# Kernel tuning notes

Measured on AMD Instinct MI355X. Metric: run time of the kernel, lower is better.

Reference implementation:

```python
import jax, jax.numpy as jnp
import numpy as np

D = 1024      # input_size
H = 16        # num_heads
HD = D // H   # head_dim
B, S = 8, 1024


def setup_inputs() -> dict:
    key = jax.random.key(0)
    ks = jax.random.split(key, 9)
    s = 1.0 / np.sqrt(D)
    return {
        "x": jax.random.normal(ks[0], (B, S, D), dtype=jnp.float32),
        "Wq": jax.random.uniform(ks[1], (D, D), jnp.float32, -s, s),
        "bq": jax.random.uniform(ks[2], (D,), jnp.float32, -s, s),
        "Wk": jax.random.uniform(ks[3], (D, D), jnp.float32, -s, s),
        "bk": jax.random.uniform(ks[4], (D,), jnp.float32, -s, s),
        "Wv": jax.random.uniform(ks[5], (D, D), jnp.float32, -s, s),
        "bv": jax.random.uniform(ks[6], (D,), jnp.float32, -s, s),
        "Wf": jax.random.uniform(ks[7], (D, D), jnp.float32, -s, s),
        "bf": jax.random.uniform(ks[8], (D,), jnp.float32, -s, s),
    }


def reference(x, Wq, bq, Wk, bk, Wv, bv, Wf, bf):
    b, s, d = x.shape
    # torch Linear: x @ W.T + b; split into heads -> [b, H, s, HD]
    def split(y):
        return y.reshape(b, s, H, HD).transpose(0, 2, 1, 3)
    q = split(x @ Wq.T + bq)
    k = split(x @ Wk.T + bk)
    v = split(x @ Wv.T + bv)
    scores = jnp.einsum("bhqd,bhkd->bhqk", q, k) / jnp.sqrt(jnp.float32(HD))
    probs = jax.nn.softmax(scores, axis=-1)
    ctx = jnp.einsum("bhqk,bhkd->bhqd", probs, v)
    ctx = ctx.transpose(0, 2, 1, 3).reshape(b, s, d)
    out = ctx @ Wf.T + bf
    return (out, probs)
```

## Files before the change

### kernel.cpp

```cpp
#include <hip/hip_runtime.h>

typedef __bf16 bf16;
typedef __bf16 bf16x4 __attribute__((ext_vector_type(4)));
typedef __bf16 bf16x8 __attribute__((ext_vector_type(8)));
typedef float  f32x4  __attribute__((ext_vector_type(4)));

constexpr int Bb = 8, Ss = 1024, Dd = 1024, Hh = 16, HDd = 64;
constexpr int Mm = Bb * Ss;
constexpr int Kk = 1024;

struct CastArgs {
  const float* src[5];
  bf16* dst[5];
  int cum[5];
};
__global__ void cast_all(CastArgs a, int tot) {
  int i = blockIdx.x * blockDim.x + threadIdx.x;
  if (i >= tot) return;
  int s, base;
  if (i < a.cum[0])      { s = 0; base = 0; }
  else if (i < a.cum[1]) { s = 1; base = a.cum[0]; }
  else if (i < a.cum[2]) { s = 2; base = a.cum[1]; }
  else if (i < a.cum[3]) { s = 3; base = a.cum[2]; }
  else                   { s = 4; base = a.cum[3]; }
  int j = i - base;
  float4 v = reinterpret_cast<const float4*>(a.src[s])[j];
  bf16x4 o = { (bf16)v.x, (bf16)v.y, (bf16)v.z, (bf16)v.w };
  reinterpret_cast<bf16x4*>(a.dst[s])[j] = o;
}

__device__ __forceinline__ void gemm_loop(const bf16* __restrict__ A, const bf16* __restrict__ Bm,
                                          int bm, int bn, unsigned char* As, unsigned char* Bs,
                                          int w, int lane, int l15, int g, f32x4 (&acc)[4][4]) {
  const int wr = (w >> 1) * 64, wc = (w & 1) * 64;
  (void)wr; (void)wc;
  const bf16* srcA[4];
  const bf16* srcB[4];
#pragma unroll
  for (int i = 0; i < 4; ++i) {
    int gch = (w * 4 + i) * 64 + lane;
    int r = gch >> 3, c = gch & 7, cs = c ^ (r & 7);
    srcA[i] = A  + (size_t)(bm * 128 + r) * Kk + cs * 8;
    srcB[i] = Bm + (size_t)(bn * 128 + r) * Kk + cs * 8;
  }
  for (int kt = 0; kt < Kk / 64; ++kt) {
    __syncthreads();
#pragma unroll
    for (int i = 0; i < 4; ++i) {
      __builtin_amdgcn_global_load_lds(
          (const __attribute__((address_space(1))) void*)(srcA[i] + kt * 64),
          (__attribute__((address_space(3))) void*)(As + (w * 4 + i) * 1024), 16, 0, 0);
      __builtin_amdgcn_global_load_lds(
          (const __attribute__((address_space(1))) void*)(srcB[i] + kt * 64),
          (__attribute__((address_space(3))) void*)(Bs + (w * 4 + i) * 1024), 16, 0, 0);
    }
    __syncthreads();
#pragma unroll
    for (int kk = 0; kk < 2; ++kk) {
      const int kb = kk * 64 + g * 16;
      bf16x8 af[4], bfr[4];
#pragma unroll
      for (int mi = 0; mi < 4; ++mi) {
        int row = ((w >> 1) * 64) + mi * 16 + l15;
        af[mi] = *reinterpret_cast<const bf16x8*>(As + row * 128 + (kb ^ ((row & 7) << 4)));
      }
#pragma unroll
      for (int ni = 0; ni < 4; ++ni) {
        int row = ((w & 1) * 64) + ni * 16 + l15;
        bfr[ni] = *reinterpret_cast<const bf16x8*>(Bs + row * 128 + (kb ^ ((row & 7) << 4)));
      }
#pragma unroll
      for (int mi = 0; mi < 4; ++mi)
#pragma unroll
        for (int ni = 0; ni < 4; ++ni)
          acc[mi][ni] = __builtin_amdgcn_mfma_f32_16x16x32_bf16(af[mi], bfr[ni], acc[mi][ni], 0, 0, 0);
    }
  }
}

__global__ __launch_bounds__(256) void gemm_qkv(const bf16* __restrict__ x,
                                                const bf16* __restrict__ wq, const bf16* __restrict__ wk,
                                                const bf16* __restrict__ wv,
                                                const float* __restrict__ bq, const float* __restrict__ bk,
                                                const float* __restrict__ bv,
                                                bf16* __restrict__ Qo, bf16* __restrict__ Ko,
                                                bf16* __restrict__ Vto) {
  const int tid = threadIdx.x;
  const int lane = tid & 63;
  const int w = tid >> 6;
  const int l15 = lane & 15, g = lane >> 4;
  const int z = blockIdx.z;

  const bf16* A; const bf16* Bm; int bm, bn;
  if (z < 2) { A = x; Bm = z ? wk : wq; bm = blockIdx.x; bn = blockIdx.y; }
  else       { A = wv; Bm = x;          bm = blockIdx.y; bn = blockIdx.x; }

  __shared__ __align__(16) unsigned char As[128 * 128];
  __shared__ __align__(16) unsigned char Bs[128 * 128];
  f32x4 acc[4][4] = {};
  gemm_loop(A, Bm, bm, bn, As, Bs, w, lane, l15, g, acc);

  const int wr = (w >> 1) * 64, wc = (w & 1) * 64;
  if (z < 2) {
    const float* bias = z ? bk : bq;
    bf16* out = z ? Ko : Qo;
    const float scale = z ? 1.f : 0.125f;
#pragma unroll
    for (int ni = 0; ni < 4; ++ni) {
      int col = bn * 128 + wc + ni * 16 + l15;
      float bv_ = bias[col];
#pragma unroll
      for (int mi = 0; mi < 4; ++mi)
#pragma unroll
        for (int r = 0; r < 4; ++r) {
          int row = bm * 128 + wr + mi * 16 + g * 4 + r;
          float val = (acc[mi][ni][r] + bv_) * scale;
          size_t adr = ((size_t)((row >> 10) * Hh + (col >> 6)) * Ss + (row & 1023)) * HDd + (col & 63);
          out[adr] = (bf16)val;
        }
    }
  } else {
#pragma unroll
    for (int mi = 0; mi < 4; ++mi)
#pragma unroll
      for (int r = 0; r < 4; ++r) {
        int row = bm * 128 + wr + mi * 16 + g * 4 + r;
        float bv_ = bv[row];
#pragma unroll
        for (int ni = 0; ni < 4; ++ni) {
          int col = bn * 128 + wc + ni * 16 + l15;
          size_t adr = ((size_t)((col >> 10) * Hh + (row >> 6)) * HDd + (row & 63)) * Ss + (col & 1023);
          Vto[adr] = (bf16)(acc[mi][ni][r] + bv_);
        }
      }
  }
}

__global__ __launch_bounds__(256) void gemm_out(const bf16* __restrict__ A, const bf16* __restrict__ Bm,
                                                const float* __restrict__ bias, float* __restrict__ out) {
  const int tid = threadIdx.x;
  const int lane = tid & 63;
  const int w = tid >> 6;
  const int l15 = lane & 15, g = lane >> 4;
  const int bn = blockIdx.x, bm = blockIdx.y;
  __shared__ __align__(16) unsigned char As[128 * 128];
  __shared__ __align__(16) unsigned char Bs[128 * 128];
  f32x4 acc[4][4] = {};
  gemm_loop(A, Bm, bm, bn, As, Bs, w, lane, l15, g, acc);
  const int wr = (w >> 1) * 64, wc = (w & 1) * 64;
#pragma unroll
  for (int ni = 0; ni < 4; ++ni) {
    int col = bn * 128 + wc + ni * 16 + l15;
    float bv_ = bias[col];
#pragma unroll
    for (int mi = 0; mi < 4; ++mi)
#pragma unroll
      for (int r = 0; r < 4; ++r) {
        int row = bm * 128 + wr + mi * 16 + g * 4 + r;
        out[(size_t)row * Dd + col] = acc[mi][ni][r] + bv_;
      }
  }
}

__global__ __launch_bounds__(512) void attn_fused(const bf16* __restrict__ Q,
                                                  const bf16* __restrict__ Kt,
                                                  const bf16* __restrict__ Vt,
                                                  float* __restrict__ probs,
                                                  bf16* __restrict__ ctx) {
  const int tid = threadIdx.x;
  const int lane = tid & 63;
  const int w = tid >> 6;
  const int l15 = lane & 15, g = lane >> 4;
  const int bh = blockIdx.x >> 3;
  const int qt = blockIdx.x & 7;
  const int q0 = qt * 128 + w * 16;

  __shared__ __align__(16) unsigned char Ks[128 * 128];
  __shared__ __align__(16) unsigned char Vs[64 * 256];
  __shared__ __align__(16) bf16 Ps[8][16][40];

  bf16x8 qf0, qf1;
  {
    const bf16* qp = Q + ((size_t)bh * Ss + q0 + l15) * HDd + g * 8;
    qf0 = *reinterpret_cast<const bf16x8*>(qp);
    qf1 = *reinterpret_cast<const bf16x8*>(qp + 32);
  }
  const bf16* kbase = Kt + (size_t)bh * Ss * HDd;
  const bf16* vbase = Vt + (size_t)bh * HDd * Ss;

  const bf16* ksrc[2];
  const bf16* vsrc[2];
#pragma unroll
  for (int i = 0; i < 2; ++i) {
    int chunk = i * 512 + tid;
    int kr = chunk >> 3, kc = (chunk & 7) ^ (kr & 7);
    ksrc[i] = kbase + (size_t)kr * HDd + kc * 8;
    int vr = chunk >> 4, vc = (chunk & 15) ^ (vr & 15);
    vsrc[i] = vbase + (size_t)vr * Ss + vc * 8;
  }

  auto kread = [&](int nk, int half) -> bf16x8 {
    int row = nk * 16 + l15;
    int chunk = (half * 4 + g) ^ (row & 7);
    return *reinterpret_cast<const bf16x8*>(Ks + row * 128 + chunk * 16);
  };
  auto vread = [&](int ni, int nkp) -> bf16x8 {
    int row = ni * 16 + l15;
    int chunk = (nkp * 4 + g) ^ (row & 15);
    return *reinterpret_cast<const bf16x8*>(Vs + row * 256 + chunk * 16);
  };

  float lr[4] = {0.f, 0.f, 0.f, 0.f};

  for (int kt = 0; kt < 8; ++kt) {
    __syncthreads();
#pragma unroll
    for (int i = 0; i < 2; ++i)
      __builtin_amdgcn_global_load_lds(
          (const __attribute__((address_space(1))) void*)(ksrc[i] + kt * 128 * HDd),
          (__attribute__((address_space(3))) void*)(Ks + (i * 512 + w * 64) * 16), 16, 0, 0);
    __syncthreads();
#pragma unroll
    for (int nk = 0; nk < 8; ++nk) {
      f32x4 sc = {0.f, 0.f, 0.f, 0.f};
      sc = __builtin_amdgcn_mfma_f32_16x16x32_bf16(qf0, kread(nk, 0), sc, 0, 0, 0);
      sc = __builtin_amdgcn_mfma_f32_16x16x32_bf16(qf1, kread(nk, 1), sc, 0, 0, 0);
#pragma unroll
      for (int r = 0; r < 4; ++r) lr[r] += __expf(sc[r]);
    }
  }
#pragma unroll
  for (int r = 0; r < 4; ++r) {
#pragma unroll
    for (int off = 1; off < 16; off <<= 1) lr[r] += __shfl_xor(lr[r], off, 64);
  }
  float rl[4];
#pragma unroll
  for (int r = 0; r < 4; ++r) rl[r] = 1.f / lr[r];

  float* prow[4];
#pragma unroll
  for (int r = 0; r < 4; ++r) prow[r] = probs + ((size_t)bh * Ss + q0 + g * 4 + r) * Ss;

  f32x4 cacc[4] = {};

  for (int kt = 0; kt < 8; ++kt) {
    __syncthreads();
#pragma unroll
    for (int i = 0; i < 2; ++i) {
      __builtin_amdgcn_global_load_lds(
          (const __attribute__((address_space(1))) void*)(ksrc[i] + kt * 128 * HDd),
          (__attribute__((address_space(3))) void*)(Ks + (i * 512 + w * 64) * 16), 16, 0, 0);
      __builtin_amdgcn_global_load_lds(
          (const __attribute__((address_space(1))) void*)(vsrc[i] + kt * 128),
          (__attribute__((address_space(3))) void*)(Vs + (i * 512 + w * 64) * 16), 16, 0, 0);
    }
    __syncthreads();
#pragma unroll
    for (int nkp = 0; nkp < 4; ++nkp) {
#pragma unroll
      for (int h = 0; h < 2; ++h) {
        int nk = nkp * 2 + h;
        f32x4 sc = {0.f, 0.f, 0.f, 0.f};
        sc = __builtin_amdgcn_mfma_f32_16x16x32_bf16(qf0, kread(nk, 0), sc, 0, 0, 0);
        sc = __builtin_amdgcn_mfma_f32_16x16x32_bf16(qf1, kread(nk, 1), sc, 0, 0, 0);
#pragma unroll
        for (int r = 0; r < 4; ++r) {
          float p = __expf(sc[r]) * rl[r];
          prow[r][kt * 128 + nk * 16 + l15] = p;
          Ps[w][g * 4 + r][h * 16 + l15] = (bf16)p;
        }
      }
      bf16x8 pf = *reinterpret_cast<const bf16x8*>(&Ps[w][l15][g * 8]);
#pragma unroll
      for (int ni = 0; ni < 4; ++ni)
        cacc[ni] = __builtin_amdgcn_mfma_f32_16x16x32_bf16(pf, vread(ni, nkp), cacc[ni], 0, 0, 0);
    }
  }

  const int bb = bh >> 4, hh = bh & 15;
#pragma unroll
  for (int ni = 0; ni < 4; ++ni)
#pragma unroll
    for (int r = 0; r < 4; ++r) {
      int q = q0 + g * 4 + r;
      ctx[((size_t)bb * Ss + q) * Dd + hh * 64 + ni * 16 + l15] = (bf16)cacc[ni][r];
    }
}

extern "C" void kernel_launch(void* const* d_in, const int* in_sizes, int n_in,
                              void* d_out, int out_size, void* d_ws, size_t ws_size,
                              hipStream_t stream) {
  (void)in_sizes; (void)n_in; (void)out_size; (void)ws_size;
  const float* x   = (const float*)d_in[0];
  const float* Wq  = (const float*)d_in[1];
  const float* bq  = (const float*)d_in[2];
  const float* Wk  = (const float*)d_in[3];
  const float* bk  = (const float*)d_in[4];
  const float* Wv  = (const float*)d_in[5];
  const float* bv  = (const float*)d_in[6];
  const float* Wf  = (const float*)d_in[7];
  const float* bfp = (const float*)d_in[8];

  char* ws = (char*)d_ws;
  size_t off = 0;
  auto alloc = [&](size_t n) { void* p = ws + off; off += (n + 255) & ~(size_t)255; return p; };
  bf16* xb   = (bf16*)alloc((size_t)Mm * Dd * 2);
  bf16* wqb  = (bf16*)alloc((size_t)Dd * Dd * 2);
  bf16* wkb  = (bf16*)alloc((size_t)Dd * Dd * 2);
  bf16* wvb  = (bf16*)alloc((size_t)Dd * Dd * 2);
  bf16* wfb  = (bf16*)alloc((size_t)Dd * Dd * 2);
  bf16* Qb   = (bf16*)alloc((size_t)Mm * Dd * 2);
  bf16* Kb   = (bf16*)alloc((size_t)Mm * Dd * 2);
  bf16* Vtb  = (bf16*)alloc((size_t)Mm * Dd * 2);
  bf16* ctxb = (bf16*)alloc((size_t)Mm * Dd * 2);

  CastArgs ca;
  ca.src[0] = x;  ca.dst[0] = xb;  int n0 = Mm * Dd / 4;
  ca.src[1] = Wq; ca.dst[1] = wqb; int nw = Dd * Dd / 4;
  ca.src[2] = Wk; ca.dst[2] = wkb;
  ca.src[3] = Wv; ca.dst[3] = wvb;
  ca.src[4] = Wf; ca.dst[4] = wfb;
  ca.cum[0] = n0; ca.cum[1] = n0 + nw; ca.cum[2] = n0 + 2 * nw;
  ca.cum[3] = n0 + 3 * nw; ca.cum[4] = n0 + 4 * nw;
  int tot = ca.cum[4];
  cast_all<<<(tot + 255) / 256, 256, 0, stream>>>(ca, tot);

  gemm_qkv<<<dim3(Mm / 128, Dd / 128, 3), 256, 0, stream>>>(xb, wqb, wkb, wvb, bq, bk, bv, Qb, Kb, Vtb);

  float* probs = (float*)d_out + (size_t)Mm * Dd;
  attn_fused<<<dim3(Bb * Hh * 8), 512, 0, stream>>>(Qb, Kb, Vtb, probs, ctxb);

  gemm_out<<<dim3(Dd / 128, Mm / 128), 256, 0, stream>>>(ctxb, wfb, bfp, (float*)d_out);
}
```

Baseline: 284.8 us.

## Double-buffer K tiles, transpose score MFMA, vectorize prob stores, read V directly

The attention kernel now double-buffers the K tile in LDS, prefetching the next tile while computing on the current one, and runs the second pass in reverse order so the last K tile from pass one is reused. The score MFMA operands are swapped so each lane holds four consecutive keys for one query row. This allows float4 stores of probabilities and bf16x4 writes into the P scratch, and reduces the row-sum reduction to two shuffles. V is no longer staged in LDS; it is loaded straight from global memory per MFMA, which saves LDS and barriers but may add global latency.

```diff
diff --git a/kernel.cpp b/kernel.cpp
--- a/kernel.cpp
+++ b/kernel.cpp
@@ -32,8 +32,6 @@
 __device__ __forceinline__ void gemm_loop(const bf16* __restrict__ A, const bf16* __restrict__ Bm,
                                           int bm, int bn, unsigned char* As, unsigned char* Bs,
                                           int w, int lane, int l15, int g, f32x4 (&acc)[4][4]) {
-  const int wr = (w >> 1) * 64, wc = (w & 1) * 64;
-  (void)wr; (void)wc;
   const bf16* srcA[4];
   const bf16* srcB[4];
 #pragma unroll
@@ -175,8 +173,7 @@
   const int qt = blockIdx.x & 7;
   const int q0 = qt * 128 + w * 16;
 
-  __shared__ __align__(16) unsigned char Ks[128 * 128];
-  __shared__ __align__(16) unsigned char Vs[64 * 256];
+  __shared__ __align__(16) unsigned char Ks[2][128 * 128];
   __shared__ __align__(16) bf16 Ps[8][16][40];
 
   bf16x8 qf0, qf1;
@@ -189,94 +186,83 @@
   const bf16* vbase = Vt + (size_t)bh * HDd * Ss;
 
   const bf16* ksrc[2];
-  const bf16* vsrc[2];
 #pragma unroll
   for (int i = 0; i < 2; ++i) {
     int chunk = i * 512 + tid;
     int kr = chunk >> 3, kc = (chunk & 7) ^ (kr & 7);
     ksrc[i] = kbase + (size_t)kr * HDd + kc * 8;
-    int vr = chunk >> 4, vc = (chunk & 15) ^ (vr & 15);
-    vsrc[i] = vbase + (size_t)vr * Ss + vc * 8;
-  }
-
-  auto kread = [&](int nk, int half) -> bf16x8 {
+  }
+
+#define STAGE_K(buf, kt)                                                                   \
+  {                                                                                        \
+    _Pragma("unroll") for (int i = 0; i < 2; ++i)                                          \
+        __builtin_amdgcn_global_load_lds(                                                  \
+            (const __attribute__((address_space(1))) void*)(ksrc[i] + (kt) * 128 * HDd),   \
+            (__attribute__((address_space(3))) void*)(Ks[buf] + (i * 512 + w * 64) * 16),  \
+            16, 0, 0);                                                                     \
+  }
+
+  auto kread = [&](int buf, int nk, int half) -> bf16x8 {
     int row = nk * 16 + l15;
     int chunk = (half * 4 + g) ^ (row & 7);
-    return *reinterpret_cast<const bf16x8*>(Ks + row * 128 + chunk * 16);
+    return *reinterpret_cast<const bf16x8*>(Ks[buf] + row * 128 + chunk * 16);
   };
-  auto vread = [&](int ni, int nkp) -> bf16x8 {
-    int row = ni * 16 + l15;
-    int chunk = (nkp * 4 + g) ^ (row & 15);
-    return *reinterpret_cast<const bf16x8*>(Vs + row * 256 + chunk * 16);
-  };
-
-  float lr[4] = {0.f, 0.f, 0.f, 0.f};
-
+
+  float lr0 = 0.f, lr1 = 0.f, lr2 = 0.f, lr3 = 0.f;
+  STAGE_K(0, 0);
+  __syncthreads();
+  int cur = 0;
   for (int kt = 0; kt < 8; ++kt) {
-    __syncthreads();
-#pragma unroll
-    for (int i = 0; i < 2; ++i)
-      __builtin_amdgcn_global_load_lds(
-          (const __attribute__((address_space(1))) void*)(ksrc[i] + kt * 128 * HDd),
-          (__attribute__((address_space(3))) void*)(Ks + (i * 512 + w * 64) * 16), 16, 0, 0);
-    __syncthreads();
+    if (kt < 7) STAGE_K(cur ^ 1, kt + 1);
 #pragma unroll
     for (int nk = 0; nk < 8; ++nk) {
       f32x4 sc = {0.f, 0.f, 0.f, 0.f};
-      sc = __builtin_amdgcn_mfma_f32_16x16x32_bf16(qf0, kread(nk, 0), sc, 0, 0, 0);
-      sc = __builtin_amdgcn_mfma_f32_16x16x32_bf16(qf1, kread(nk, 1), sc, 0, 0, 0);
-#pragma unroll
-      for (int r = 0; r < 4; ++r) lr[r] += __expf(sc[r]);
-    }
-  }
-#pragma unroll
-  for (int r = 0; r < 4; ++r) {
-#pragma unroll
-    for (int off = 1; off < 16; off <<= 1) lr[r] += __shfl_xor(lr[r], off, 64);
-  }
-  float rl[4];
-#pragma unroll
-  for (int r = 0; r < 4; ++r) rl[r] = 1.f / lr[r];
-
-  float* prow[4];
-#pragma unroll
-  for (int r = 0; r < 4; ++r) prow[r] = probs + ((size_t)bh * Ss + q0 + g * 4 + r) * Ss;
-
+      sc = __builtin_amdgcn_mfma_f32_16x16x32_bf16(kread(cur, nk, 0), qf0, sc, 0, 0, 0);
+      sc = __builtin_amdgcn_mfma_f32_16x16x32_bf16(kread(cur, nk, 1), qf1, sc, 0, 0, 0);
+      lr0 += __expf(sc[0]); lr1 += __expf(sc[1]);
+      lr2 += __expf(sc[2]); lr3 += __expf(sc[3]);
+    }
+    __syncthreads();
+    cur ^= 1;
+  }
+  float lsum = (lr0 + lr1) + (lr2 + lr3);
+  lsum += __shfl_xor(lsum, 16, 64);
+  lsum += __shfl_xor(lsum, 32, 64);
+  const float rl = 1.f / lsum;
+
+  float* const prow = probs + ((size_t)bh * Ss + q0 + l15) * Ss;
   f32x4 cacc[4] = {};
 
-  for (int kt = 0; kt < 8; ++kt) {
-    __syncthreads();
-#pragma unroll
-    for (int i = 0; i < 2; ++i) {
-      __builtin_amdgcn_global_load_lds(
-          (const __attribute__((address_space(1))) void*)(ksrc[i] + kt * 128 * HDd),
-          (__attribute__((address_space(3))) void*)(Ks + (i * 512 + w * 64) * 16), 16, 0, 0);
-      __builtin_amdgcn_global_load_lds(
-          (const __attribute__((address_space(1))) void*)(vsrc[i] + kt * 128),
-          (__attribute__((address_space(3))) void*)(Vs + (i * 512 + w * 64) * 16), 16, 0, 0);
-    }
-    __syncthreads();
+  cur = 1;
+  for (int kt = 7; kt >= 0; --kt) {
+    if (kt > 0) STAGE_K(cur ^ 1, kt - 1);
 #pragma unroll
     for (int nkp = 0; nkp < 4; ++nkp) {
 #pragma unroll
       for (int h = 0; h < 2; ++h) {
         int nk = nkp * 2 + h;
         f32x4 sc = {0.f, 0.f, 0.f, 0.f};
-        sc = __builtin_amdgcn_mfma_f32_16x16x32_bf16(qf0, kread(nk, 0), sc, 0, 0, 0);
-        sc = __builtin_amdgcn_mfma_f32_16x16x32_bf16(qf1, kread(nk, 1), sc, 0, 0, 0);
-#pragma unroll
-        for (int r = 0; r < 4; ++r) {
-          float p = __expf(sc[r]) * rl[r];
-          prow[r][kt * 128 + nk * 16 + l15] = p;
-          Ps[w][g * 4 + r][h * 16 + l15] = (bf16)p;
-        }
+        sc = __builtin_amdgcn_mfma_f32_16x16x32_bf16(kread(cur, nk, 0), qf0, sc, 0, 0, 0);
+        sc = __builtin_amdgcn_mfma_f32_16x16x32_bf16(kread(cur, nk, 1), qf1, sc, 0, 0, 0);
+        f32x4 pv;
+#pragma unroll
+        for (int r = 0; r < 4; ++r) pv[r] = __expf(sc[r]) * rl;
+        *reinterpret_cast<f32x4*>(prow + kt * 128 + nk * 16 + g * 4) = pv;
+        bf16x4 pb = { (bf16)pv[0], (bf16)pv[1], (bf16)pv[2], (bf16)pv[3] };
+        *reinterpret_cast<bf16x4*>(&Ps[w][l15][h * 16 + g * 4]) = pb;
       }
       bf16x8 pf = *reinterpret_cast<const bf16x8*>(&Ps[w][l15][g * 8]);
 #pragma unroll
-      for (int ni = 0; ni < 4; ++ni)
-        cacc[ni] = __builtin_amdgcn_mfma_f32_16x16x32_bf16(pf, vread(ni, nkp), cacc[ni], 0, 0, 0);
-    }
-  }
+      for (int ni = 0; ni < 4; ++ni) {
+        bf16x8 vf = *reinterpret_cast<const bf16x8*>(
+            vbase + (size_t)(ni * 16 + l15) * Ss + kt * 128 + nkp * 32 + g * 8);
+        cacc[ni] = __builtin_amdgcn_mfma_f32_16x16x32_bf16(pf, vf, cacc[ni], 0, 0, 0);
+      }
+    }
+    __syncthreads();
+    cur ^= 1;
+  }
+#undef STAGE_K
 
   const int bb = bh >> 4, hh = bh & 15;
 #pragma unroll
```

After: 343.7 us. 1.21x slower.
